# Kernel optimization log

Measured on AMD Instinct MI355X. Metric: run time of the kernel, lower is better.

## Reference

```python
import jax, jax.numpy as jnp
import numpy as np

N_NODES = 50000
N_EDGES = 800000
IN_FEATS = 128
OUT_FEATS = 128


def setup_inputs() -> dict:
    key = jax.random.key(0)
    k1, k2, k3, k4, k5 = jax.random.split(key, 5)
    feature = jax.random.normal(k1, (N_NODES, IN_FEATS), dtype=jnp.float32)
    src_idx = jax.random.randint(k2, (N_EDGES,), 0, N_NODES, dtype=jnp.int32)
    dst_idx = jax.random.randint(k3, (N_EDGES,), 0, N_NODES, dtype=jnp.int32)
    # nn.Linear(in, out): weight [out, in], bias [out]
    bound = 1.0 / np.sqrt(IN_FEATS)
    W = jax.random.uniform(k4, (OUT_FEATS, IN_FEATS), minval=-bound, maxval=bound, dtype=jnp.float32)
    b = jax.random.uniform(k5, (OUT_FEATS,), minval=-bound, maxval=bound, dtype=jnp.float32)
    return {"feature": feature, "src_idx": src_idx, "dst_idx": dst_idx, "W": W, "b": b}


def reference(feature, src_idx, dst_idx, W, b):
    # message: copy src node feature along each edge; reduce: sum into dst node
    msgs = feature[src_idx]                                   # [E, F_in] gather
    agg = jax.ops.segment_sum(msgs, dst_idx, num_segments=N_NODES)  # [N, F_in]
    # apply: linear + relu
    h = jax.nn.relu(agg @ W.T + b)                            # [N, F_out]
    return h
```

## Files before the change

kernel.cpp:

```cpp
#include <hip/hip_runtime.h>
#include <hip/hip_fp16.h>

#define F 128
#define TILE 256
#define TSH 8
#define CHUNK 4096
#define BCAP 8192
#define ROWS2 32
#define LINB 256
#define SCAN_TILE 1024

__device__ inline float4 h8_to_f4(uint2 u) {
    union { unsigned int x; __half2 h; } a, b;
    a.x = u.x; b.x = u.y;
    const float2 lo = __half22float2(a.h);
    const float2 hi = __half22float2(b.h);
    return make_float4(lo.x, lo.y, hi.x, hi.y);
}

__global__ __launch_bounds__(256) void prep_count_kernel(
        const float* __restrict__ feat, unsigned int* __restrict__ featH,
        const float* __restrict__ W, __half* __restrict__ wTh,
        int* __restrict__ offsets, const int* __restrict__ dst,
        int* __restrict__ blkCnt,
        int N, int NF4, int E, int NT, int NCHUNK) {
    __shared__ int h[256];
    const int tid = threadIdx.x;
    const int bid = blockIdx.x;
    if (bid < NCHUNK) {
        h[tid] = 0;
        __syncthreads();
        const int e0 = bid * CHUNK;
        const int n = min(CHUNK, E - e0);
        for (int i = tid; i < n; i += 256) atomicAdd(&h[dst[e0 + i] >> TSH], 1);
        __syncthreads();
        if (tid < NT) blkCnt[(size_t)tid * NCHUNK + bid] = h[tid];
    } else {
        const int i = (bid - NCHUNK) * 256 + tid;
        if (i < NF4) {
            const float4 v = ((const float4*)feat)[i];
            union { __half2 h2; unsigned int u; } a, b;
            a.h2 = __floats2half2_rn(v.x, v.y);
            b.h2 = __floats2half2_rn(v.z, v.w);
            ((uint2*)featH)[i] = make_uint2(a.u, b.u);
        }
        if (i < F * F) {
            int o = i >> 7, k = i & 127;
            wTh[k * F + o] = __float2half(W[i]);
        }
        if (i == 0 && (N & (TILE - 1)) == 0) offsets[N] = 0;
    }
}

__global__ __launch_bounds__(256) void binA_scan_kernel(
        const int* __restrict__ blkCnt, int* __restrict__ blkOff,
        int* __restrict__ bucketBase, int E, int NT, int NCHUNK) {
    __shared__ int red[256];
    const int t = blockIdx.x;
    const int tid = threadIdx.x;

    const int lim = t * NCHUNK;
    int s = 0;
    for (int i = tid; i < lim; i += 256) s += blkCnt[i];
    red[tid] = s;
    __syncthreads();
    for (int off = 128; off > 0; off >>= 1) {
        if (tid < off) red[tid] += red[tid + off];
        __syncthreads();
    }
    const int base = red[0];
    __syncthreads();

    int carry = base;
    for (int c0 = 0; c0 < NCHUNK; c0 += 256) {
        const int b = c0 + tid;
        const int v = (b < NCHUNK) ? blkCnt[(size_t)t * NCHUNK + b] : 0;
        red[tid] = v;
        __syncthreads();
        for (int off = 1; off < 256; off <<= 1) {
            int tv = (tid >= off) ? red[tid - off] : 0;
            __syncthreads();
            red[tid] += tv;
            __syncthreads();
        }
        const int excl = red[tid] - v;
        if (b < NCHUNK) blkOff[(size_t)t * NCHUNK + b] = carry + excl;
        const int tot = red[255];
        __syncthreads();
        carry += tot;
    }
    if (tid == 0) {
        bucketBase[t] = base;
        if (t == 0) bucketBase[NT] = E;
    }
}

__global__ __launch_bounds__(256) void binA_scatter_kernel(
        const int* __restrict__ src, const int* __restrict__ dst,
        const int* __restrict__ blkOff,
        unsigned int* __restrict__ edgebuf, int E, int NT, int NCHUNK) {
    __shared__ int h[256];
    __shared__ int lds2[256];
    __shared__ int cstart[256];
    __shared__ uint2 stage[CHUNK];
    const int tid = threadIdx.x, b = blockIdx.x;
    h[tid] = 0;
    __syncthreads();
    const int e0 = b * CHUNK;
    const int n = min(CHUNK, E - e0);
    for (int i = tid; i < n; i += 256) atomicAdd(&h[dst[e0 + i] >> TSH], 1);
    __syncthreads();
    const int myc = h[tid];
    lds2[tid] = myc;
    __syncthreads();
    for (int off = 1; off < 256; off <<= 1) {
        int t = (tid >= off) ? lds2[tid - off] : 0;
        __syncthreads();
        lds2[tid] += t;
        __syncthreads();
    }
    const int runstart = lds2[tid] - myc;
    if (tid < NT) cstart[tid] = blkOff[(size_t)tid * NCHUNK + b] - runstart;
    h[tid] = runstart;
    __syncthreads();
    for (int i = tid; i < n; i += 256) {
        const int e = e0 + i;
        const int d = dst[e];
        const int p = atomicAdd(&h[d >> TSH], 1);
        stage[p] = make_uint2((unsigned)src[e], (unsigned)d);
    }
    __syncthreads();
    for (int i = tid; i < n; i += 256) {
        const uint2 v = stage[i];
        const int t = (int)v.y >> TSH;
        edgebuf[cstart[t] + i] = (v.x << 8) | (v.y & 255u);
    }
}

__global__ __launch_bounds__(256) void build_tile_kernel(
        const unsigned int* __restrict__ edgebuf, const int* __restrict__ bucketBase,
        int* __restrict__ offsets, int* __restrict__ ssrc, int N, int NT) {
    __shared__ int h[TILE];
    __shared__ int excl[TILE];
    __shared__ int stage[BCAP];
    const int t = blockIdx.x, tid = threadIdx.x;
    const int s0 = bucketBase[t], s1 = bucketBase[t + 1];
    const int cnt = s1 - s0;
    const int n0 = t << TSH;
    const int n1 = min(n0 + TILE, N);
    h[tid] = 0;
    __syncthreads();
    for (int i = tid; i < cnt; i += 256)
        atomicAdd(&h[(int)(edgebuf[s0 + i] & 255u)], 1);
    __syncthreads();
    const int myv = h[tid];
    excl[tid] = myv;
    __syncthreads();
    for (int off = 1; off < 256; off <<= 1) {
        int tv = (tid >= off) ? excl[tid - off] : 0;
        __syncthreads();
        excl[tid] += tv;
        __syncthreads();
    }
    const int ex = excl[tid] - myv;
    const int v = n0 + tid;
    if (v < n1) offsets[v] = ex;
    if (tid == 255 && n1 == N && (N & (TILE - 1)) != 0) offsets[N] = excl[255];
    h[tid] = ex;
    __syncthreads();
    if (cnt <= BCAP) {
        for (int i = tid; i < cnt; i += 256) {
            const unsigned int e = edgebuf[s0 + i];
            const int p = atomicAdd(&h[(int)(e & 255u)], 1);
            stage[p] = (int)(e >> 8);
        }
        __syncthreads();
        for (int i = tid; i < cnt; i += 256) ssrc[s0 + i] = stage[i];
    } else {
        for (int i = tid; i < cnt; i += 256) {
            const unsigned int e = edgebuf[s0 + i];
            const int p = atomicAdd(&h[(int)(e & 255u)], 1);
            ssrc[s0 + p] = (int)(e >> 8);
        }
    }
}

__global__ __launch_bounds__(256) void agg16_kernel(
        const uint4* __restrict__ fH,
        const int* __restrict__ ssrc,
        const int* __restrict__ offs,
        const int* __restrict__ base,
        float* __restrict__ out, int N) {
    const int gwave = (blockIdx.x * blockDim.x + threadIdx.x) >> 6;
    const int lane = threadIdx.x & 63;
    const int g = lane >> 4;
    const int q = lane & 15;
    const int nwaves = (gridDim.x * blockDim.x) >> 6;

    for (int v = gwave; v < N; v += nwaves) {
        const int s0 = offs[v] + base[v >> TSH];
        const int s1 = offs[v + 1] + base[(v + 1) >> TSH];
        float a[8];
#pragma unroll
        for (int j = 0; j < 8; ++j) a[j] = 0.f;

        int e = s0 + g;
        for (; e + 4 < s1; e += 8) {
            const int i0 = ssrc[e], i1 = ssrc[e + 4];
            const uint4 u0 = fH[(size_t)i0 * 16 + q];
            const uint4 u1 = fH[(size_t)i1 * 16 + q];
            {
                union { unsigned int u; __half2 h; } c0, c1, c2, c3;
                c0.u = u0.x; c1.u = u0.y; c2.u = u0.z; c3.u = u0.w;
                const float2 f0 = __half22float2(c0.h);
                const float2 f1 = __half22float2(c1.h);
                const float2 f2 = __half22float2(c2.h);
                const float2 f3 = __half22float2(c3.h);
                a[0] += f0.x; a[1] += f0.y; a[2] += f1.x; a[3] += f1.y;
                a[4] += f2.x; a[5] += f2.y; a[6] += f3.x; a[7] += f3.y;
            }
            {
                union { unsigned int u; __half2 h; } c0, c1, c2, c3;
                c0.u = u1.x; c1.u = u1.y; c2.u = u1.z; c3.u = u1.w;
                const float2 f0 = __half22float2(c0.h);
                const float2 f1 = __half22float2(c1.h);
                const float2 f2 = __half22float2(c2.h);
                const float2 f3 = __half22float2(c3.h);
                a[0] += f0.x; a[1] += f0.y; a[2] += f1.x; a[3] += f1.y;
                a[4] += f2.x; a[5] += f2.y; a[6] += f3.x; a[7] += f3.y;
            }
        }
        for (; e < s1; e += 4) {
            const uint4 u0 = fH[(size_t)ssrc[e] * 16 + q];
            union { unsigned int u; __half2 h; } c0, c1, c2, c3;
            c0.u = u0.x; c1.u = u0.y; c2.u = u0.z; c3.u = u0.w;
            const float2 f0 = __half22float2(c0.h);
            const float2 f1 = __half22float2(c1.h);
            const float2 f2 = __half22float2(c2.h);
            const float2 f3 = __half22float2(c3.h);
            a[0] += f0.x; a[1] += f0.y; a[2] += f1.x; a[3] += f1.y;
            a[4] += f2.x; a[5] += f2.y; a[6] += f3.x; a[7] += f3.y;
        }

#pragma unroll
        for (int j = 0; j < 8; ++j) {
            a[j] += __shfl_xor(a[j], 16);
            a[j] += __shfl_xor(a[j], 32);
        }
        if (g == 0) {
            float4* orow = (float4*)(out + (size_t)v * F);
            float4 r0, r1;
            r0.x = a[0]; r0.y = a[1]; r0.z = a[2]; r0.w = a[3];
            r1.x = a[4]; r1.y = a[5]; r1.z = a[6]; r1.w = a[7];
            orow[q * 2] = r0;
            orow[q * 2 + 1] = r1;
        }
    }
}

__global__ __launch_bounds__(LINB) void linear_relu_kernel(
        float* __restrict__ h, const __half* __restrict__ wTh,
        const float* __restrict__ b, int N) {
    __shared__ __align__(16) float sA[ROWS2][132];
    const int tid = threadIdx.x;
    const int row0 = blockIdx.x * ROWS2;

    for (int i = tid; i < ROWS2 * 32; i += LINB) {
        int r = i >> 5, q = i & 31;
        int gr = row0 + r;
        float4 v = make_float4(0.f, 0.f, 0.f, 0.f);
        if (gr < N) v = ((const float4*)(h + (size_t)gr * F))[q];
        *((float4*)&sA[r][q << 2]) = v;
    }
    __syncthreads();

    const int tr = tid >> 5;
    const int tc = tid & 31;
    float acc[4][4];
#pragma unroll
    for (int i = 0; i < 4; ++i)
#pragma unroll
        for (int j = 0; j < 4; ++j) acc[i][j] = 0.f;

    const uint2* wTh2 = (const uint2*)wTh;
    uint2 u0 = wTh2[0 * 32 + tc];
    uint2 u1 = wTh2[1 * 32 + tc];
    uint2 u2 = wTh2[2 * 32 + tc];
    uint2 u3 = wTh2[3 * 32 + tc];

#pragma unroll 1
    for (int k = 0; k < F - 4; k += 4) {
        const uint2 p0 = wTh2[(k + 4) * 32 + tc];
        const uint2 p1 = wTh2[(k + 5) * 32 + tc];
        const uint2 p2 = wTh2[(k + 6) * 32 + tc];
        const uint2 p3 = wTh2[(k + 7) * 32 + tc];
        const float4 w0 = h8_to_f4(u0);
        const float4 w1 = h8_to_f4(u1);
        const float4 w2 = h8_to_f4(u2);
        const float4 w3 = h8_to_f4(u3);
#pragma unroll
        for (int i = 0; i < 4; ++i) {
            const float4 a = *(const float4*)&sA[tr * 4 + i][k];
            acc[i][0] += a.x * w0.x + a.y * w1.x + a.z * w2.x + a.w * w3.x;
            acc[i][1] += a.x * w0.y + a.y * w1.y + a.z * w2.y + a.w * w3.y;
            acc[i][2] += a.x * w0.z + a.y * w1.z + a.z * w2.z + a.w * w3.z;
            acc[i][3] += a.x * w0.w + a.y * w1.w + a.z * w2.w + a.w * w3.w;
        }
        u0 = p0; u1 = p1; u2 = p2; u3 = p3;
    }
    {
        const int k = F - 4;
        const float4 w0 = h8_to_f4(u0);
        const float4 w1 = h8_to_f4(u1);
        const float4 w2 = h8_to_f4(u2);
        const float4 w3 = h8_to_f4(u3);
#pragma unroll
        for (int i = 0; i < 4; ++i) {
            const float4 a = *(const float4*)&sA[tr * 4 + i][k];
            acc[i][0] += a.x * w0.x + a.y * w1.x + a.z * w2.x + a.w * w3.x;
            acc[i][1] += a.x * w0.y + a.y * w1.y + a.z * w2.y + a.w * w3.y;
            acc[i][2] += a.x * w0.z + a.y * w1.z + a.z * w2.z + a.w * w3.z;
            acc[i][3] += a.x * w0.w + a.y * w1.w + a.z * w2.w + a.w * w3.w;
        }
    }

    const float4 bias = ((const float4*)b)[tc];
#pragma unroll
    for (int i = 0; i < 4; ++i) {
        int gr = row0 + tr * 4 + i;
        if (gr < N) {
            float4 o;
            o.x = fmaxf(acc[i][0] + bias.x, 0.f);
            o.y = fmaxf(acc[i][1] + bias.y, 0.f);
            o.z = fmaxf(acc[i][2] + bias.z, 0.f);
            o.w = fmaxf(acc[i][3] + bias.w, 0.f);
            ((float4*)(h + (size_t)gr * F))[tc] = o;
        }
    }
}

__global__ void prep2_kernel(const float* __restrict__ W, __half* __restrict__ wTh,
                             int* __restrict__ counts, int N) {
    int i = blockIdx.x * 256 + threadIdx.x;
    if (i < F * F) {
        int o = i >> 7, k = i & 127;
        wTh[k * F + o] = __float2half(W[i]);
    }
    if (i < N) counts[i] = 0;
}

__global__ void hist_kernel(const int* __restrict__ dst, int* __restrict__ counts, int E) {
    int e = blockIdx.x * blockDim.x + threadIdx.x;
    if (e < E) atomicAdd(&counts[dst[e]], 1);
}

__global__ __launch_bounds__(256) void scan1_kernel(const int* __restrict__ counts,
                                                    int* __restrict__ offsets,
                                                    int* __restrict__ cursor,
                                                    int* __restrict__ blockSums, int N) {
    __shared__ int lds[256];
    const int tid = threadIdx.x;
    const int i0 = blockIdx.x * SCAN_TILE + tid * 4;
    int v[4];
    int s = 0;
#pragma unroll
    for (int j = 0; j < 4; ++j) {
        int i = i0 + j;
        v[j] = (i < N) ? counts[i] : 0;
        s += v[j];
    }
    lds[tid] = s;
    __syncthreads();
    for (int off = 1; off < 256; off <<= 1) {
        int t = (tid >= off) ? lds[tid - off] : 0;
        __syncthreads();
        lds[tid] += t;
        __syncthreads();
    }
    int excl = lds[tid] - s;
#pragma unroll
    for (int j = 0; j < 4; ++j) {
        int i = i0 + j;
        if (i < N) {
            offsets[i] = excl;
            cursor[i] = excl;
        } else if (i == N) {
            offsets[N] = excl;
        }
        excl += v[j];
    }
    if (tid == 255) blockSums[blockIdx.x] = lds[255];
}

__global__ __launch_bounds__(256) void scan2_kernel(int* __restrict__ blockSums,
                                                    int* __restrict__ offsets,
                                                    int NB, int N) {
    __shared__ int lds[256];
    const int tid = threadIdx.x;
    int s = (tid < NB) ? blockSums[tid] : 0;
    lds[tid] = s;
    __syncthreads();
    for (int off = 1; off < 256; off <<= 1) {
        int t = (tid >= off) ? lds[tid - off] : 0;
        __syncthreads();
        lds[tid] += t;
        __syncthreads();
    }
    if (tid < NB) blockSums[tid] = lds[tid] - s;
    if (tid == NB && NB < 256) blockSums[NB] = lds[255];
    if (tid == 0 && (N & (SCAN_TILE - 1)) == 0) offsets[N] = 0;
}

__global__ void place_kernel(const int* __restrict__ src, const int* __restrict__ dst,
                             int* __restrict__ cursor, const int* __restrict__ base,
                             int* __restrict__ ssrc, int E) {
    int e = blockIdx.x * blockDim.x + threadIdx.x;
    if (e < E) {
        int d = dst[e];
        int pos = atomicAdd(&cursor[d], 1) + base[d >> 10];
        ssrc[pos] = src[e];
    }
}

__global__ __launch_bounds__(256) void agg_kernel(const float* __restrict__ feat,
                                                  const int* __restrict__ ssrc,
                                                  const int* __restrict__ offs,
                                                  const int* __restrict__ base,
                                                  float* __restrict__ out, int N) {
    const int gwave = (blockIdx.x * blockDim.x + threadIdx.x) >> 6;
    const int lane = threadIdx.x & 63;
    const int half = lane >> 5;
    const int q = lane & 31;
    const int nwaves = (gridDim.x * blockDim.x) >> 6;
    const float4* feat4 = (const float4*)feat;
    for (int v = gwave; v < N; v += nwaves) {
        const int s0 = offs[v] + base[v >> 10];
        const int s1 = offs[v + 1] + base[(v + 1) >> 10];
        float ax = 0.f, ay = 0.f, az = 0.f, aw = 0.f;
        int e = s0 + half;
        for (; e + 6 < s1; e += 8) {
            int i0 = ssrc[e], i1 = ssrc[e + 2], i2 = ssrc[e + 4], i3 = ssrc[e + 6];
            const float4 f0 = feat4[(size_t)i0 * 32 + q];
            const float4 f1 = feat4[(size_t)i1 * 32 + q];
            const float4 f2 = feat4[(size_t)i2 * 32 + q];
            const float4 f3 = feat4[(size_t)i3 * 32 + q];
            ax += (f0.x + f1.x) + (f2.x + f3.x);
            ay += (f0.y + f1.y) + (f2.y + f3.y);
            az += (f0.z + f1.z) + (f2.z + f3.z);
            aw += (f0.w + f1.w) + (f2.w + f3.w);
        }
        for (; e < s1; e += 2) {
            const float4 f0 = feat4[(size_t)ssrc[e] * 32 + q];
            ax += f0.x; ay += f0.y; az += f0.z; aw += f0.w;
        }
        ax += __shfl_xor(ax, 32);
        ay += __shfl_xor(ay, 32);
        az += __shfl_xor(az, 32);
        aw += __shfl_xor(aw, 32);
        if (half == 0) {
            float4 r;
            r.x = ax; r.y = ay; r.z = az; r.w = aw;
            ((float4*)(out + (size_t)v * F))[q] = r;
        }
    }
}

__global__ void zero_f4_kernel(float4* __restrict__ out, int n4) {
    int i = blockIdx.x * blockDim.x + threadIdx.x;
    if (i < n4) out[i] = make_float4(0.f, 0.f, 0.f, 0.f);
}

__global__ void scatter_atomic_kernel(const float* __restrict__ feat,
                                      const int* __restrict__ src,
                                      const int* __restrict__ dst,
                                      float* __restrict__ agg, int E) {
    int gid = blockIdx.x * blockDim.x + threadIdx.x;
    int e = gid >> 5;
    if (e >= E) return;
    int q = gid & 31;
    int s = src[e];
    int d = dst[e];
    const float4 v = ((const float4*)(feat + (size_t)s * F))[q];
    float* o = agg + (size_t)d * F + (q << 2);
    atomicAdd(o + 0, v.x);
    atomicAdd(o + 1, v.y);
    atomicAdd(o + 2, v.z);
    atomicAdd(o + 3, v.w);
}

__global__ __launch_bounds__(256) void linear_relu_w_kernel(
        float* __restrict__ h, const float* __restrict__ W,
        const float* __restrict__ b, int N) {
    __shared__ __align__(16) float sA[64][132];
    const int tid = threadIdx.x;
    const int row0 = blockIdx.x * 64;

    for (int i = tid; i < 64 * 32; i += 256) {
        int r = i >> 5, q = i & 31;
        int gr = row0 + r;
        float4 v = make_float4(0.f, 0.f, 0.f, 0.f);
        if (gr < N) v = ((const float4*)(h + (size_t)gr * F))[q];
        *((float4*)&sA[r][q << 2]) = v;
    }
    __syncthreads();

    const int tr = tid >> 5;
    const int tc = tid & 31;
    float acc[8][4];
#pragma unroll
    for (int i = 0; i < 8; ++i)
#pragma unroll
        for (int j = 0; j < 4; ++j) acc[i][j] = 0.f;

    const float* Wr0 = W + (size_t)(tc * 4 + 0) * F;
    const float* Wr1 = W + (size_t)(tc * 4 + 1) * F;
    const float* Wr2 = W + (size_t)(tc * 4 + 2) * F;
    const float* Wr3 = W + (size_t)(tc * 4 + 3) * F;

    for (int k = 0; k < F; k += 4) {
        const float4 w0 = *(const float4*)&Wr0[k];
        const float4 w1 = *(const float4*)&Wr1[k];
        const float4 w2 = *(const float4*)&Wr2[k];
        const float4 w3 = *(const float4*)&Wr3[k];
#pragma unroll
        for (int i = 0; i < 8; ++i) {
            const float4 a = *(const float4*)&sA[tr * 8 + i][k];
            acc[i][0] += a.x * w0.x + a.y * w0.y + a.z * w0.z + a.w * w0.w;
            acc[i][1] += a.x * w1.x + a.y * w1.y + a.z * w1.z + a.w * w1.w;
            acc[i][2] += a.x * w2.x + a.y * w2.y + a.z * w2.z + a.w * w2.w;
            acc[i][3] += a.x * w3.x + a.y * w3.y + a.z * w3.z + a.w * w3.w;
        }
    }

    const float4 bias = ((const float4*)b)[tc];
#pragma unroll
    for (int i = 0; i < 8; ++i) {
        int gr = row0 + tr * 8 + i;
        if (gr < N) {
            float4 o;
            o.x = fmaxf(acc[i][0] + bias.x, 0.f);
            o.y = fmaxf(acc[i][1] + bias.y, 0.f);
            o.z = fmaxf(acc[i][2] + bias.z, 0.f);
            o.w = fmaxf(acc[i][3] + bias.w, 0.f);
            ((float4*)(h + (size_t)gr * F))[tc] = o;
        }
    }
}

extern "C" void kernel_launch(void* const* d_in, const int* in_sizes, int n_in,
                              void* d_out, int out_size, void* d_ws, size_t ws_size,
                              hipStream_t stream) {
    const float* feat = (const float*)d_in[0];
    const int*   src  = (const int*)d_in[1];
    const int*   dst  = (const int*)d_in[2];
    const float* W    = (const float*)d_in[3];
    const float* b    = (const float*)d_in[4];
    float* out = (float*)d_out;

    const int N = in_sizes[0] / F;
    const int E = in_sizes[1];
    const int NT = (N + TILE - 1) / TILE;
    const int NCHUNK = (E + CHUNK - 1) / CHUNK;
    const int NB = (N + SCAN_TILE - 1) / SCAN_TILE;

    auto align4 = [](size_t x) { return (x + 3) & ~(size_t)3; };

    const size_t o_featH = 0;
    const size_t o_wTh   = align4(o_featH + (size_t)N * 64);
    const size_t o_offs  = align4(o_wTh + (size_t)(F * F) / 2);
    const size_t o_bb    = align4(o_offs + (size_t)N + 1);
    const size_t o_blk   = align4(o_bb + (size_t)NT + 1);
    const size_t o_boff  = align4(o_blk + (size_t)NT * NCHUNK);
    const size_t o_ebuf  = align4(o_boff + (size_t)NT * NCHUNK);
    const size_t o_ssrc  = align4(o_ebuf + (size_t)E);
    const size_t need_main = (o_ssrc + (size_t)E) * sizeof(int);

    const size_t csr_ints = (size_t)(F * F) / 2 + N + (N + 1) + N + 260 + E;
    const size_t need_mid = csr_ints * sizeof(int);
    const bool nb_ok = (NB < 256) || ((N & (SCAN_TILE - 1)) != 0 && NB <= 256);

    if (ws_size >= need_main && NT <= 256 && N < (1 << 24)) {
        unsigned int* featH = (unsigned int*)d_ws;
        __half* wTh          = (__half*)((int*)d_ws + o_wTh);
        int* offsets         = (int*)d_ws + o_offs;
        int* bucketBase      = (int*)d_ws + o_bb;
        int* blkCnt          = (int*)d_ws + o_blk;
        int* blkOff          = (int*)d_ws + o_boff;
        unsigned int* edgebuf = (unsigned int*)((int*)d_ws + o_ebuf);
        int* ssrc            = (int*)d_ws + o_ssrc;

        const int NF4 = N * 32;
        const int nprep = (NF4 + 255) / 256;
        prep_count_kernel<<<NCHUNK + nprep, 256, 0, stream>>>(
            feat, featH, W, wTh, offsets, dst, blkCnt, N, NF4, E, NT, NCHUNK);
        binA_scan_kernel<<<NT, 256, 0, stream>>>(blkCnt, blkOff, bucketBase, E, NT, NCHUNK);
        binA_scatter_kernel<<<NCHUNK, 256, 0, stream>>>(src, dst, blkOff, edgebuf, E, NT, NCHUNK);
        build_tile_kernel<<<NT, 256, 0, stream>>>(edgebuf, bucketBase, offsets, ssrc, N, NT);
        agg16_kernel<<<2048, 256, 0, stream>>>((const uint4*)featH, ssrc, offsets, bucketBase, out, N);
        linear_relu_kernel<<<(N + ROWS2 - 1) / ROWS2, LINB, 0, stream>>>(out, wTh, b, N);
    } else if (ws_size >= need_mid && nb_ok) {
        __half* wTh    = (__half*)d_ws;
        int* counts    = (int*)d_ws + (F * F) / 2;
        int* offsets   = counts + N;
        int* cursor    = offsets + (N + 1);
        int* blockSums = cursor + N;
        int* ssrc      = blockSums + 260;

        prep2_kernel<<<(N + 255) / 256, 256, 0, stream>>>(W, wTh, counts, N);
        hist_kernel<<<(E + 255) / 256, 256, 0, stream>>>(dst, counts, E);
        scan1_kernel<<<NB, 256, 0, stream>>>(counts, offsets, cursor, blockSums, N);
        scan2_kernel<<<1, 256, 0, stream>>>(blockSums, offsets, NB, N);
        place_kernel<<<(E + 255) / 256, 256, 0, stream>>>(src, dst, cursor, blockSums, ssrc, E);
        agg_kernel<<<2048, 256, 0, stream>>>(feat, ssrc, offsets, blockSums, out, N);
        linear_relu_kernel<<<(N + ROWS2 - 1) / ROWS2, LINB, 0, stream>>>(out, wTh, b, N);
    } else {
        const int n4 = N * (F / 4);
        zero_f4_kernel<<<(n4 + 255) / 256, 256, 0, stream>>>((float4*)out, n4);
        const int sthreads = E * 32;
        scatter_atomic_kernel<<<(sthreads + 255) / 256, 256, 0, stream>>>(feat, src, dst, out, E);
        linear_relu_w_kernel<<<(N + 63) / 64, 256, 0, stream>>>(out, W, b, N);
    }
}
```

Before: 200.6 us.

## Replace FP32 linear layer with MFMA f16 matmul on half-precision aggregates

The aggregation kernel now writes its per-node sums as fp16 into a workspace buffer instead of fp32 rows in the output. A new MFMA-based linear kernel multiplies these fp16 rows by an fp16 copy of W, stored untransposed. It uses 16x16x32 f16 matrix instructions with fp32 accumulation and writes bias+ReLU directly to the output. This is meant to cut the scalar-FMA cost of the dense layer and halve the intermediate traffic, at the cost of rounding the aggregated sums to fp16 before the matmul.

After: 180.3 us. -10.1%, faster.

```diff
diff --git a/kernel.cpp b/kernel.cpp
--- a/kernel.cpp
+++ b/kernel.cpp
@@ -10,6 +10,9 @@
 #define LINB 256
 #define SCAN_TILE 1024
 
+typedef _Float16 f16x8 __attribute__((ext_vector_type(8)));
+typedef float f32x4 __attribute__((ext_vector_type(4)));
+
 __device__ inline float4 h8_to_f4(uint2 u) {
     union { unsigned int x; __half2 h; } a, b;
     a.x = u.x; b.x = u.y;
@@ -20,7 +23,7 @@
 
 __global__ __launch_bounds__(256) void prep_count_kernel(
         const float* __restrict__ feat, unsigned int* __restrict__ featH,
-        const float* __restrict__ W, __half* __restrict__ wTh,
+        const float* __restrict__ W, __half* __restrict__ woh,
         int* __restrict__ offsets, const int* __restrict__ dst,
         int* __restrict__ blkCnt,
         int N, int NF4, int E, int NT, int NCHUNK) {
@@ -44,10 +47,7 @@
             b.h2 = __floats2half2_rn(v.z, v.w);
             ((uint2*)featH)[i] = make_uint2(a.u, b.u);
         }
-        if (i < F * F) {
-            int o = i >> 7, k = i & 127;
-            wTh[k * F + o] = __float2half(W[i]);
-        }
+        if (i < F * F) woh[i] = __float2half(W[i]);
         if (i == 0 && (N & (TILE - 1)) == 0) offsets[N] = 0;
     }
 }
@@ -190,7 +190,7 @@
         const int* __restrict__ ssrc,
         const int* __restrict__ offs,
         const int* __restrict__ base,
-        float* __restrict__ out, int N) {
+        uint4* __restrict__ aggH, int N) {
     const int gwave = (blockIdx.x * blockDim.x + threadIdx.x) >> 6;
     const int lane = threadIdx.x & 63;
     const int g = lane >> 4;
@@ -248,93 +248,54 @@
             a[j] += __shfl_xor(a[j], 32);
         }
         if (g == 0) {
-            float4* orow = (float4*)(out + (size_t)v * F);
-            float4 r0, r1;
-            r0.x = a[0]; r0.y = a[1]; r0.z = a[2]; r0.w = a[3];
-            r1.x = a[4]; r1.y = a[5]; r1.z = a[6]; r1.w = a[7];
-            orow[q * 2] = r0;
-            orow[q * 2 + 1] = r1;
-        }
-    }
-}
-
-__global__ __launch_bounds__(LINB) void linear_relu_kernel(
-        float* __restrict__ h, const __half* __restrict__ wTh,
-        const float* __restrict__ b, int N) {
-    __shared__ __align__(16) float sA[ROWS2][132];
+            union { __half2 h2; unsigned int u; } p0, p1, p2, p3;
+            p0.h2 = __floats2half2_rn(a[0], a[1]);
+            p1.h2 = __floats2half2_rn(a[2], a[3]);
+            p2.h2 = __floats2half2_rn(a[4], a[5]);
+            p3.h2 = __floats2half2_rn(a[6], a[7]);
+            aggH[(size_t)v * 16 + q] = make_uint4(p0.u, p1.u, p2.u, p3.u);
+        }
+    }
+}
+
+__global__ __launch_bounds__(256) void linear_mfma_kernel(
+        const uint4* __restrict__ aggH,
+        const uint4* __restrict__ woh4,
+        const float* __restrict__ bias,
+        float* __restrict__ out, int N) {
     const int tid = threadIdx.x;
-    const int row0 = blockIdx.x * ROWS2;
-
-    for (int i = tid; i < ROWS2 * 32; i += LINB) {
-        int r = i >> 5, q = i & 31;
-        int gr = row0 + r;
-        float4 v = make_float4(0.f, 0.f, 0.f, 0.f);
-        if (gr < N) v = ((const float4*)(h + (size_t)gr * F))[q];
-        *((float4*)&sA[r][q << 2]) = v;
-    }
-    __syncthreads();
-
-    const int tr = tid >> 5;
-    const int tc = tid & 31;
-    float acc[4][4];
-#pragma unroll
-    for (int i = 0; i < 4; ++i)
-#pragma unroll
-        for (int j = 0; j < 4; ++j) acc[i][j] = 0.f;
-
-    const uint2* wTh2 = (const uint2*)wTh;
-    uint2 u0 = wTh2[0 * 32 + tc];
-    uint2 u1 = wTh2[1 * 32 + tc];
-    uint2 u2 = wTh2[2 * 32 + tc];
-    uint2 u3 = wTh2[3 * 32 + tc];
-
-#pragma unroll 1
-    for (int k = 0; k < F - 4; k += 4) {
-        const uint2 p0 = wTh2[(k + 4) * 32 + tc];
-        const uint2 p1 = wTh2[(k + 5) * 32 + tc];
-        const uint2 p2 = wTh2[(k + 6) * 32 + tc];
-        const uint2 p3 = wTh2[(k + 7) * 32 + tc];
-        const float4 w0 = h8_to_f4(u0);
-        const float4 w1 = h8_to_f4(u1);
-        const float4 w2 = h8_to_f4(u2);
-        const float4 w3 = h8_to_f4(u3);
-#pragma unroll
-        for (int i = 0; i < 4; ++i) {
-            const float4 a = *(const float4*)&sA[tr * 4 + i][k];
-            acc[i][0] += a.x * w0.x + a.y * w1.x + a.z * w2.x + a.w * w3.x;
-            acc[i][1] += a.x * w0.y + a.y * w1.y + a.z * w2.y + a.w * w3.y;
-            acc[i][2] += a.x * w0.z + a.y * w1.z + a.z * w2.z + a.w * w3.z;
-            acc[i][3] += a.x * w0.w + a.y * w1.w + a.z * w2.w + a.w * w3.w;
-        }
-        u0 = p0; u1 = p1; u2 = p2; u3 = p3;
-    }
-    {
-        const int k = F - 4;
-        const float4 w0 = h8_to_f4(u0);
-        const float4 w1 = h8_to_f4(u1);
-        const float4 w2 = h8_to_f4(u2);
-        const float4 w3 = h8_to_f4(u3);
-#pragma unroll
-        for (int i = 0; i < 4; ++i) {
-            const float4 a = *(const float4*)&sA[tr * 4 + i][k];
-            acc[i][0] += a.x * w0.x + a.y * w1.x + a.z * w2.x + a.w * w3.x;
-            acc[i][1] += a.x * w0.y + a.y * w1.y + a.z * w2.y + a.w * w3.y;
-            acc[i][2] += a.x * w0.z + a.y * w1.z + a.z * w2.z + a.w * w3.z;
-            acc[i][3] += a.x * w0.w + a.y * w1.w + a.z * w2.w + a.w * w3.w;
-        }
-    }
-
-    const float4 bias = ((const float4*)b)[tc];
-#pragma unroll
-    for (int i = 0; i < 4; ++i) {
-        int gr = row0 + tr * 4 + i;
-        if (gr < N) {
-            float4 o;
-            o.x = fmaxf(acc[i][0] + bias.x, 0.f);
-            o.y = fmaxf(acc[i][1] + bias.y, 0.f);
-            o.z = fmaxf(acc[i][2] + bias.z, 0.f);
-            o.w = fmaxf(acc[i][3] + bias.w, 0.f);
-            ((float4*)(h + (size_t)gr * F))[tc] = o;
+    const int wid = tid >> 6;
+    const int lane = tid & 63;
+    const int m16 = lane & 15;
+    const int kq = lane >> 4;
+    const int row0 = blockIdx.x * 64 + wid * 16;
+    const int rowA = row0 + m16;
+
+    union U { uint4 u; f16x8 h; };
+    U af[4];
+    if (rowA < N) {
+        const uint4* r = aggH + (size_t)rowA * 16 + kq;
+        af[0].u = r[0]; af[1].u = r[4]; af[2].u = r[8]; af[3].u = r[12];
+    } else {
+        af[0].u = af[1].u = af[2].u = af[3].u = make_uint4(0u, 0u, 0u, 0u);
+    }
+
+#pragma unroll
+    for (int g = 0; g < 8; ++g) {
+        const uint4* wrow = woh4 + (size_t)(g * 16 + m16) * 16 + kq;
+        U b0, b1, b2, b3;
+        b0.u = wrow[0]; b1.u = wrow[4]; b2.u = wrow[8]; b3.u = wrow[12];
+        f32x4 acc = {0.f, 0.f, 0.f, 0.f};
+        acc = __builtin_amdgcn_mfma_f32_16x16x32_f16(af[0].h, b0.h, acc, 0, 0, 0);
+        acc = __builtin_amdgcn_mfma_f32_16x16x32_f16(af[1].h, b1.h, acc, 0, 0, 0);
+        acc = __builtin_amdgcn_mfma_f32_16x16x32_f16(af[2].h, b2.h, acc, 0, 0, 0);
+        acc = __builtin_amdgcn_mfma_f32_16x16x32_f16(af[3].h, b3.h, acc, 0, 0, 0);
+        const float bv = bias[g * 16 + m16];
+#pragma unroll
+        for (int r = 0; r < 4; ++r) {
+            const int gr = row0 + kq * 4 + r;
+            if (gr < N)
+                out[(size_t)gr * F + g * 16 + m16] = fmaxf(acc[r] + bv, 0.f);
         }
     }
 }
@@ -465,6 +426,87 @@
     }
 }
 
+__global__ __launch_bounds__(LINB) void linear_relu_kernel(
+        float* __restrict__ h, const __half* __restrict__ wTh,
+        const float* __restrict__ b, int N) {
+    __shared__ __align__(16) float sA[ROWS2][132];
+    const int tid = threadIdx.x;
+    const int row0 = blockIdx.x * ROWS2;
+
+    for (int i = tid; i < ROWS2 * 32; i += LINB) {
+        int r = i >> 5, q = i & 31;
+        int gr = row0 + r;
+        float4 v = make_float4(0.f, 0.f, 0.f, 0.f);
+        if (gr < N) v = ((const float4*)(h + (size_t)gr * F))[q];
+        *((float4*)&sA[r][q << 2]) = v;
+    }
+    __syncthreads();
+
+    const int tr = tid >> 5;
+    const int tc = tid & 31;
+    float acc[4][4];
+#pragma unroll
+    for (int i = 0; i < 4; ++i)
+#pragma unroll
+        for (int j = 0; j < 4; ++j) acc[i][j] = 0.f;
+
+    const uint2* wTh2 = (const uint2*)wTh;
+    uint2 u0 = wTh2[0 * 32 + tc];
+    uint2 u1 = wTh2[1 * 32 + tc];
+    uint2 u2 = wTh2[2 * 32 + tc];
+    uint2 u3 = wTh2[3 * 32 + tc];
+
+#pragma unroll 1
+    for (int k = 0; k < F - 4; k += 4) {
+        const uint2 p0 = wTh2[(k + 4) * 32 + tc];
+        const uint2 p1 = wTh2[(k + 5) * 32 + tc];
+        const uint2 p2 = wTh2[(k + 6) * 32 + tc];
+        const uint2 p3 = wTh2[(k + 7) * 32 + tc];
+        const float4 w0 = h8_to_f4(u0);
+        const float4 w1 = h8_to_f4(u1);
+        const float4 w2 = h8_to_f4(u2);
+        const float4 w3 = h8_to_f4(u3);
+#pragma unroll
+        for (int i = 0; i < 4; ++i) {
+            const float4 a = *(const float4*)&sA[tr * 4 + i][k];
+            acc[i][0] += a.x * w0.x + a.y * w1.x + a.z * w2.x + a.w * w3.x;
+            acc[i][1] += a.x * w0.y + a.y * w1.y + a.z * w2.y + a.w * w3.y;
+            acc[i][2] += a.x * w0.z + a.y * w1.z + a.z * w2.z + a.w * w3.z;
+            acc[i][3] += a.x * w0.w + a.y * w1.w + a.z * w2.w + a.w * w3.w;
+        }
+        u0 = p0; u1 = p1; u2 = p2; u3 = p3;
+    }
+    {
+        const int k = F - 4;
+        const float4 w0 = h8_to_f4(u0);
+        const float4 w1 = h8_to_f4(u1);
+        const float4 w2 = h8_to_f4(u2);
+        const float4 w3 = h8_to_f4(u3);
+#pragma unroll
+        for (int i = 0; i < 4; ++i) {
+            const float4 a = *(const float4*)&sA[tr * 4 + i][k];
+            acc[i][0] += a.x * w0.x + a.y * w1.x + a.z * w2.x + a.w * w3.x;
+            acc[i][1] += a.x * w0.y + a.y * w1.y + a.z * w2.y + a.w * w3.y;
+            acc[i][2] += a.x * w0.z + a.y * w1.z + a.z * w2.z + a.w * w3.z;
+            acc[i][3] += a.x * w0.w + a.y * w1.w + a.z * w2.w + a.w * w3.w;
+        }
+    }
+
+    const float4 bias = ((const float4*)b)[tc];
+#pragma unroll
+    for (int i = 0; i < 4; ++i) {
+        int gr = row0 + tr * 4 + i;
+        if (gr < N) {
+            float4 o;
+            o.x = fmaxf(acc[i][0] + bias.x, 0.f);
+            o.y = fmaxf(acc[i][1] + bias.y, 0.f);
+            o.z = fmaxf(acc[i][2] + bias.z, 0.f);
+            o.w = fmaxf(acc[i][3] + bias.w, 0.f);
+            ((float4*)(h + (size_t)gr * F))[tc] = o;
+        }
+    }
+}
+
 __global__ void zero_f4_kernel(float4* __restrict__ out, int n4) {
     int i = blockIdx.x * blockDim.x + threadIdx.x;
     if (i < n4) out[i] = make_float4(0.f, 0.f, 0.f, 0.f);
@@ -566,8 +608,9 @@
     auto align4 = [](size_t x) { return (x + 3) & ~(size_t)3; };
 
     const size_t o_featH = 0;
-    const size_t o_wTh   = align4(o_featH + (size_t)N * 64);
-    const size_t o_offs  = align4(o_wTh + (size_t)(F * F) / 2);
+    const size_t o_aggH  = align4(o_featH + (size_t)N * 64);
+    const size_t o_woh   = align4(o_aggH + (size_t)N * 64);
+    const size_t o_offs  = align4(o_woh + (size_t)(F * F) / 2);
     const size_t o_bb    = align4(o_offs + (size_t)N + 1);
     const size_t o_blk   = align4(o_bb + (size_t)NT + 1);
     const size_t o_boff  = align4(o_blk + (size_t)NT * NCHUNK);
@@ -581,7 +624,8 @@
 
     if (ws_size >= need_main && NT <= 256 && N < (1 << 24)) {
         unsigned int* featH = (unsigned int*)d_ws;
-        __half* wTh          = (__half*)((int*)d_ws + o_wTh);
+        uint4* aggH          = (uint4*)((int*)d_ws + o_aggH);
+        __half* woh          = (__half*)((int*)d_ws + o_woh);
         int* offsets         = (int*)d_ws + o_offs;
         int* bucketBase      = (int*)d_ws + o_bb;
         int* blkCnt          = (int*)d_ws + o_blk;
@@ -592,12 +636,13 @@
         const int NF4 = N * 32;
         const int nprep = (NF4 + 255) / 256;
         prep_count_kernel<<<NCHUNK + nprep, 256, 0, stream>>>(
-            feat, featH, W, wTh, offsets, dst, blkCnt, N, NF4, E, NT, NCHUNK);
+            feat, featH, W, woh, offsets, dst, blkCnt, N, NF4, E, NT, NCHUNK);
         binA_scan_kernel<<<NT, 256, 0, stream>>>(blkCnt, blkOff, bucketBase, E, NT, NCHUNK);
         binA_scatter_kernel<<<NCHUNK, 256, 0, stream>>>(src, dst, blkOff, edgebuf, E, NT, NCHUNK);
         build_tile_kernel<<<NT, 256, 0, stream>>>(edgebuf, bucketBase, offsets, ssrc, N, NT);
-        agg16_kernel<<<2048, 256, 0, stream>>>((const uint4*)featH, ssrc, offsets, bucketBase, out, N);
-        linear_relu_kernel<<<(N + ROWS2 - 1) / ROWS2, LINB, 0, stream>>>(out, wTh, b, N);
+        agg16_kernel<<<2048, 256, 0, stream>>>((const uint4*)featH, ssrc, offsets, bucketBase, aggH, N);
+        linear_mfma_kernel<<<(N + 63) / 64, 256, 0, stream>>>(
+            (const uint4*)aggH, (const uint4*)woh, b, out, N);
     } else if (ws_size >= need_mid && nb_ok) {
         __half* wTh    = (__half*)d_ws;
         int* counts    = (int*)d_ws + (F * F) / 2;
```
